# Optimization experiments

Measured on AMD Instinct MI355X. Metric: run time of the kernel, lower is better.

Reference implementation:

```python
import jax, jax.numpy as jnp
import numpy as np

B, T, D, H, HS = 256, 256, 384, 6, 64  # batch, seq (=block_size), n_embd, n_heads, head_size


def setup_inputs() -> dict:
    key = jax.random.key(0)
    k0, k1, k2 = jax.random.split(key, 3)
    x = jax.random.normal(k0, (B, T, D), dtype=jnp.float32)
    # per-head qkv weights, stacked: [H, n_embd, 3*head_size] (x @ W layout)
    W_qkv = jax.random.normal(k1, (H, D, 3 * HS), dtype=jnp.float32) * 0.02
    W_out = jax.random.normal(k2, (H * HS, D), dtype=jnp.float32) * 0.02
    b_out = jnp.zeros((D,), dtype=jnp.float32)
    return {"x": x, "W_qkv": W_qkv, "W_out": W_out, "b_out": b_out}


def reference(x, W_qkv, W_out, b_out):
    # Eval-mode (dropout disabled). Vectorized over heads instead of the
    # original Python loop; identical math per head.
    b, t, d = x.shape
    h, hs3 = W_qkv.shape[0], W_qkv.shape[2]
    hs = hs3 // 3
    qkv = jnp.einsum('btd,hde->bhte', x, W_qkv)  # [B,H,T,3*HS]
    q, k, v = jnp.split(qkv, 3, axis=-1)  # each [B,H,T,HS]
    scale = 1.0 / jnp.sqrt(jnp.asarray(hs, dtype=x.dtype))
    wei = jnp.einsum('bhte,bhse->bhts', q, k) * scale  # [B,H,T,T]
    causal = jnp.tril(jnp.ones((t, t), dtype=bool))
    wei = jnp.where(causal, wei, -jnp.inf)
    wei = jax.nn.softmax(wei, axis=-1)
    out = jnp.einsum('bhts,bhse->bhte', wei, v)  # [B,H,T,HS]
    out = out.transpose(0, 2, 1, 3).reshape(b, t, h * hs)  # concat heads
    return out @ W_out + b_out
```

## Files before the change

### kernel.cpp

```cpp
#include <hip/hip_runtime.h>


typedef __attribute__((ext_vector_type(8))) short short8;
typedef __attribute__((ext_vector_type(4))) float f32x4;

#define NBATCH 256
#define NT 256
#define ND 384
#define NH 6
#define NHS 64

__device__ __forceinline__ unsigned short f2bf(float f) {
  unsigned int u = __float_as_uint(f);
  u += 0x7fffu + ((u >> 16) & 1u);
  return (unsigned short)(u >> 16);
}

__device__ __forceinline__ unsigned int cvtpk(float lo, float hi) {
  unsigned int r;
  asm("v_cvt_pk_bf16_f32 %0, %1, %2" : "=v"(r) : "v"(lo), "v"(hi));
  return r;
}

__device__ __forceinline__ ushort4 pack4(f32x4 v) {
  union { uint2 u; ushort4 s; } r;
  r.u.x = cvtpk(v[0], v[1]);
  r.u.y = cvtpk(v[2], v[3]);
  return r.s;
}

__device__ __forceinline__ void gload16(const void* g, void* l) {
  __builtin_amdgcn_global_load_lds(
      (const __attribute__((address_space(1))) void*)g,
      (__attribute__((address_space(3))) void*)l, 16, 0, 0);
}

__global__ __launch_bounds__(256) void prep_all(const float* __restrict__ x,
                                                const float* __restrict__ Wqkv,
                                                const float* __restrict__ Wout,
                                                unsigned short* __restrict__ xb,
                                                unsigned short* __restrict__ Wqt,
                                                unsigned short* __restrict__ Wot) {
  const int bid = blockIdx.x;
  if (bid < 12288) {
    size_t i = ((size_t)bid * 256 + threadIdx.x) * 8;
    float4 a = *reinterpret_cast<const float4*>(&x[i]);
    float4 b = *reinterpret_cast<const float4*>(&x[i + 4]);
    ushort4 lo, hi;
    lo.x = f2bf(a.x); lo.y = f2bf(a.y); lo.z = f2bf(a.z); lo.w = f2bf(a.w);
    hi.x = f2bf(b.x); hi.y = f2bf(b.y); hi.z = f2bf(b.z); hi.w = f2bf(b.w);
    *reinterpret_cast<ushort4*>(&xb[i]) = lo;
    *reinterpret_cast<ushort4*>(&xb[i + 4]) = hi;
  } else if (bid < 14016) {
    int idx = (bid - 12288) * 256 + threadIdx.x;
    int h = idx / (192 * ND);
    int rem = idx % (192 * ND);
    int e = rem / ND;
    int d = rem % ND;
    float v = Wqkv[((size_t)h * ND + d) * 192 + e];
    if (e < 64) v *= 0.125f * 1.44269504088896340736f;
    Wqt[idx] = f2bf(v);
  } else {
    int idx = (bid - 14016) * 256 + threadIdx.x;
    int n = idx / ND;
    int k = idx % ND;
    Wot[idx] = f2bf(Wout[(size_t)k * ND + n]);
  }
}

__global__ __launch_bounds__(256, 2) void qkv_gemm(const unsigned short* __restrict__ xb,
                                                   const unsigned short* __restrict__ Wt,
                                                   unsigned short* __restrict__ Qb,
                                                   unsigned short* __restrict__ Kb,
                                                   unsigned short* __restrict__ Vtb) {
  __shared__ __align__(16) unsigned short As[2][128 * 64];
  __shared__ __align__(16) unsigned short Bs[2][192 * 64];
  const int tid = threadIdx.x;
  const int lane = tid & 63, w = tid >> 6;
  const int l15 = lane & 15, lg = lane >> 4;
  const int wm = w >> 1, wn = w & 1;

  const int bid = blockIdx.x;
  const int xcd = bid & 7, pos = bid >> 3;
  const int h = pos % 6;
  const int mt = xcd * 64 + pos / 6;
  const int m0 = mt * 128;
  const unsigned short* Wh = Wt + (size_t)h * 192 * ND;

  f32x4 acc[4][6];
#pragma unroll
  for (int i = 0; i < 4; i++)
#pragma unroll
    for (int j = 0; j < 6; j++) acc[i][j] = (f32x4){0.f, 0.f, 0.f, 0.f};

  int arow[4], acsw[4], brow[6], bcsw[6];
#pragma unroll
  for (int j = 0; j < 4; j++) {
    int chunk = j * 256 + tid;
    arow[j] = chunk >> 3;
    acsw[j] = (chunk & 7) ^ (arow[j] & 7);
  }
#pragma unroll
  for (int j = 0; j < 6; j++) {
    int chunk = j * 256 + tid;
    brow[j] = chunk >> 3;
    bcsw[j] = (chunk & 7) ^ (brow[j] & 7);
  }

#define STAGE(nb, k0)                                                              \
  do {                                                                             \
    _Pragma("unroll") for (int j = 0; j < 4; j++)                                  \
        gload16(&xb[(size_t)(m0 + arow[j]) * ND + (k0) + acsw[j] * 8],             \
                &As[nb][(j * 256 + w * 64) * 8]);                                  \
    _Pragma("unroll") for (int j = 0; j < 6; j++)                                  \
        gload16(&Wh[(size_t)brow[j] * ND + (k0) + bcsw[j] * 8],                    \
                &Bs[nb][(j * 256 + w * 64) * 8]);                                  \
  } while (0)

  STAGE(0, 0);
  __syncthreads();

  int cur = 0;
  for (int kt = 0; kt < 6; ++kt) {
    if (kt < 5) STAGE(cur ^ 1, (kt + 1) * 64);
    short8 af[4][2], bf[6][2];
#pragma unroll
    for (int mi = 0; mi < 4; mi++) {
      const int row = wm * 64 + mi * 16 + l15;
#pragma unroll
      for (int kk = 0; kk < 2; kk++)
        af[mi][kk] = *reinterpret_cast<const short8*>(
            &As[cur][row * 64 + (((kk * 4 + lg) ^ (row & 7)) * 8)]);
    }
#pragma unroll
    for (int ni = 0; ni < 6; ni++) {
      const int row = wn * 96 + ni * 16 + l15;
#pragma unroll
      for (int kk = 0; kk < 2; kk++)
        bf[ni][kk] = *reinterpret_cast<const short8*>(
            &Bs[cur][row * 64 + (((kk * 4 + lg) ^ (row & 7)) * 8)]);
    }
#pragma unroll
    for (int kk = 0; kk < 2; kk++)
#pragma unroll
      for (int mi = 0; mi < 4; mi++)
#pragma unroll
        for (int ni = 0; ni < 6; ni++)
          acc[mi][ni] = __builtin_amdgcn_mfma_f32_16x16x32_bf16(af[mi][kk], bf[ni][kk], acc[mi][ni], 0, 0, 0);
    __syncthreads();
    cur ^= 1;
  }

  const int b = m0 >> 8, t0 = m0 & 255;
  const size_t bh = (size_t)b * NH + h;
#pragma unroll
  for (int mi = 0; mi < 4; mi++)
#pragma unroll
    for (int ni = 0; ni < 6; ni++) {
      const int col = wn * 96 + ni * 16 + l15;
      const int p = col >> 6, e = col & 63;
      const int mr = wm * 64 + mi * 16 + lg * 4;
      if (p == 2) {
        *reinterpret_cast<ushort4*>(&Vtb[(bh * 64 + e) * NT + t0 + mr]) = pack4(acc[mi][ni]);
      } else {
        unsigned short* dst = (p == 0) ? Qb : Kb;
        size_t base = (bh * NT + t0 + mr) * 64 + e;
#pragma unroll
        for (int r = 0; r < 4; r++) dst[base + (size_t)r * 64] = f2bf(acc[mi][ni][r]);
      }
    }
#undef STAGE
}

__global__ __launch_bounds__(256, 2) void attn_fwd(const unsigned short* __restrict__ Qb,
                                                   const unsigned short* __restrict__ Kb,
                                                   const unsigned short* __restrict__ Vtb,
                                                   unsigned short* __restrict__ AO) {
  __shared__ __align__(16) unsigned short Ks[256 * 64];
  __shared__ __align__(16) unsigned short Plds[4][32 * 64];
  const int bh = blockIdx.x;
  const int tid = threadIdx.x;
  const int w = tid >> 6, lane = tid & 63;
  const int l15 = lane & 15, lg = lane >> 4;
  const unsigned short* Qh = Qb + (size_t)bh * NT * 64;
  const unsigned short* Kh = Kb + (size_t)bh * NT * 64;
  const unsigned short* Vh = Vtb + (size_t)bh * 64 * NT;
  unsigned short* P = Plds[w];
  const int swz = (l15 & 7) << 3;

  short8 qf[2][2];
  {
    const int q0 = w * 32;
#pragma unroll
    for (int mi = 0; mi < 2; mi++)
#pragma unroll
      for (int kb = 0; kb < 2; kb++)
        qf[mi][kb] = *reinterpret_cast<const short8*>(
            &Qh[(size_t)(q0 + mi * 16 + l15) * 64 + kb * 32 + lg * 8]);
  }

#pragma unroll
  for (int j = 0; j < 8; j++) {
    const int c = j * 256 + tid;
    const int row = c >> 3, cc = c & 7;
    gload16(&Kh[(size_t)row * 64 + ((cc ^ (row & 7)) * 8)], &Ks[c * 8]);
  }
  __syncthreads();

  const int b = bh / NH, h = bh % NH;

#pragma unroll
  for (int pass = 0; pass < 2; ++pass) {
    const int qt = pass ? (7 - w) : w;
    const int q0 = qt * 32;

    if (pass) {
#pragma unroll
      for (int mi = 0; mi < 2; mi++)
#pragma unroll
        for (int kb = 0; kb < 2; kb++)
          qf[mi][kb] = *reinterpret_cast<const short8*>(
              &Qh[(size_t)(q0 + mi * 16 + l15) * 64 + kb * 32 + lg * 8]);
    }

    f32x4 ot[4][2];
#pragma unroll
    for (int i = 0; i < 4; i++)
#pragma unroll
      for (int j = 0; j < 2; j++) ot[i][j] = (f32x4){0.f, 0.f, 0.f, 0.f};
    float mrun[2] = {-3e38f, -3e38f}, lsum[2] = {0.f, 0.f};

    const int nch = (qt >> 1) + 1;
    for (int ch = 0; ch < nch; ++ch) {
      const int kv0 = ch * 64;
      short8 va[4][2];
#pragma unroll
      for (int erb = 0; erb < 4; erb++) {
        const int row = erb * 16 + l15;
        va[erb][0] = *reinterpret_cast<const short8*>(&Vh[(size_t)row * NT + kv0 + lg * 8]);
        va[erb][1] = *reinterpret_cast<const short8*>(&Vh[(size_t)row * NT + kv0 + 32 + lg * 8]);
      }

      f32x4 st[4][2];
#pragma unroll
      for (int i = 0; i < 4; i++)
#pragma unroll
        for (int j = 0; j < 2; j++) st[i][j] = (f32x4){0.f, 0.f, 0.f, 0.f};
      __builtin_amdgcn_s_setprio(1);
#pragma unroll
      for (int ni = 0; ni < 4; ni++) {
        const int row = kv0 + ni * 16 + l15;
        const short8 kf0 = *reinterpret_cast<const short8*>(
            &Ks[row * 64 + ((lg ^ (row & 7)) * 8)]);
        const short8 kf1 = *reinterpret_cast<const short8*>(
            &Ks[row * 64 + (((4 + lg) ^ (row & 7)) * 8)]);
#pragma unroll
        for (int mi = 0; mi < 2; mi++) {
          st[ni][mi] = __builtin_amdgcn_mfma_f32_16x16x32_bf16(kf0, qf[mi][0], st[ni][mi], 0, 0, 0);
          st[ni][mi] = __builtin_amdgcn_mfma_f32_16x16x32_bf16(kf1, qf[mi][1], st[ni][mi], 0, 0, 0);
        }
      }
      __builtin_amdgcn_s_setprio(0);

      if (ch == nch - 1) {
#pragma unroll
        for (int ni = 0; ni < 4; ni++)
#pragma unroll
          for (int mi = 0; mi < 2; mi++)
#pragma unroll
            for (int r = 0; r < 4; r++)
              if (kv0 + ni * 16 + lg * 4 + r > q0 + mi * 16 + l15)
                st[ni][mi][r] = -1e30f;
      }

#pragma unroll
      for (int mi = 0; mi < 2; mi++) {
        float tmax = st[0][mi][0];
#pragma unroll
        for (int ni = 0; ni < 4; ni++)
#pragma unroll
          for (int r = 0; r < 4; r++) tmax = fmaxf(tmax, st[ni][mi][r]);
        tmax = fmaxf(tmax, __shfl_xor(tmax, 16));
        tmax = fmaxf(tmax, __shfl_xor(tmax, 32));
        if (__any(tmax > mrun[mi] + 8.0f)) {
          const float mnew = fmaxf(mrun[mi], tmax);
          const float corr = __builtin_amdgcn_exp2f(mrun[mi] - mnew);
          lsum[mi] *= corr;
#pragma unroll
          for (int erb = 0; erb < 4; erb++)
#pragma unroll
            for (int r = 0; r < 4; r++) ot[erb][mi][r] *= corr;
          mrun[mi] = mnew;
        }
        const float mref = mrun[mi];
        float ls = 0.f;
        const int prow = (mi * 16 + l15) * 64;
#pragma unroll
        for (int ni = 0; ni < 4; ni++) {
          const float p0 = __builtin_amdgcn_exp2f(st[ni][mi][0] - mref);
          const float p1 = __builtin_amdgcn_exp2f(st[ni][mi][1] - mref);
          const float p2 = __builtin_amdgcn_exp2f(st[ni][mi][2] - mref);
          const float p3 = __builtin_amdgcn_exp2f(st[ni][mi][3] - mref);
          ls += (p0 + p1) + (p2 + p3);
          uint2 wv;
          wv.x = cvtpk(p0, p1);
          wv.y = cvtpk(p2, p3);
          *reinterpret_cast<uint2*>(&P[prow + ((ni * 16 + lg * 4) ^ swz)]) = wv;
        }
        ls += __shfl_xor(ls, 16);
        ls += __shfl_xor(ls, 32);
        lsum[mi] += ls;
      }

      short8 pb[2][2];
#pragma unroll
      for (int kk = 0; kk < 2; kk++)
#pragma unroll
        for (int mi = 0; mi < 2; mi++)
          pb[kk][mi] = *reinterpret_cast<const short8*>(
              &P[(mi * 16 + l15) * 64 + ((kk * 32 + lg * 8) ^ swz)]);
      __builtin_amdgcn_s_setprio(1);
#pragma unroll
      for (int erb = 0; erb < 4; erb++)
#pragma unroll
        for (int mi = 0; mi < 2; mi++) {
          ot[erb][mi] = __builtin_amdgcn_mfma_f32_16x16x32_bf16(va[erb][0], pb[0][mi], ot[erb][mi], 0, 0, 0);
          ot[erb][mi] = __builtin_amdgcn_mfma_f32_16x16x32_bf16(va[erb][1], pb[1][mi], ot[erb][mi], 0, 0, 0);
        }
      __builtin_amdgcn_s_setprio(0);
    }

#pragma unroll
    for (int mi = 0; mi < 2; mi++) {
      const float rl = 1.0f / lsum[mi];
      const int q = q0 + mi * 16 + l15;
#pragma unroll
      for (int erb = 0; erb < 4; erb++) {
        f32x4 v;
#pragma unroll
        for (int r = 0; r < 4; r++) v[r] = ot[erb][mi][r] * rl;
        *reinterpret_cast<ushort4*>(&AO[((size_t)(b * NT + q)) * ND + h * 64 + erb * 16 + lg * 4]) =
            pack4(v);
      }
    }
  }
}

__global__ __launch_bounds__(256, 2) void out_gemm(const unsigned short* __restrict__ AO,
                                                   const unsigned short* __restrict__ Wot,
                                                   const float* __restrict__ bout,
                                                   float* __restrict__ out) {
  __shared__ __align__(16) unsigned short As[2][128 * 64];
  __shared__ __align__(16) unsigned short Bs[2][192 * 64];
  const int tid = threadIdx.x;
  const int lane = tid & 63, w = tid >> 6;
  const int l15 = lane & 15, lg = lane >> 4;
  const int wm = w >> 1, wn = w & 1;

  const int bid = blockIdx.x;
  const int xcd = bid & 7, pos = bid >> 3;
  const int n0 = (pos & 1) * 192;
  const int m0 = (xcd * 64 + (pos >> 1)) * 128;
  const unsigned short* Wh = Wot + (size_t)n0 * ND;

  f32x4 acc[4][6];
#pragma unroll
  for (int i = 0; i < 4; i++)
#pragma unroll
    for (int j = 0; j < 6; j++) acc[i][j] = (f32x4){0.f, 0.f, 0.f, 0.f};

  int arow[4], acsw[4], brow[6], bcsw[6];
#pragma unroll
  for (int j = 0; j < 4; j++) {
    int chunk = j * 256 + tid;
    arow[j] = chunk >> 3;
    acsw[j] = (chunk & 7) ^ (arow[j] & 7);
  }
#pragma unroll
  for (int j = 0; j < 6; j++) {
    int chunk = j * 256 + tid;
    brow[j] = chunk >> 3;
    bcsw[j] = (chunk & 7) ^ (brow[j] & 7);
  }

#define STAGE(nb, k0)                                                              \
  do {                                                                             \
    _Pragma("unroll") for (int j = 0; j < 4; j++)                                  \
        gload16(&AO[(size_t)(m0 + arow[j]) * ND + (k0) + acsw[j] * 8],             \
                &As[nb][(j * 256 + w * 64) * 8]);                                  \
    _Pragma("unroll") for (int j = 0; j < 6; j++)                                  \
        gload16(&Wh[(size_t)brow[j] * ND + (k0) + bcsw[j] * 8],                    \
                &Bs[nb][(j * 256 + w * 64) * 8]);                                  \
  } while (0)

  STAGE(0, 0);
  __syncthreads();

  int cur = 0;
  for (int kt = 0; kt < 6; ++kt) {
    if (kt < 5) STAGE(cur ^ 1, (kt + 1) * 64);
    short8 af[4][2], bf[6][2];
#pragma unroll
    for (int mi = 0; mi < 4; mi++) {
      const int row = wm * 64 + mi * 16 + l15;
#pragma unroll
      for (int kk = 0; kk < 2; kk++)
        af[mi][kk] = *reinterpret_cast<const short8*>(
            &As[cur][row * 64 + (((kk * 4 + lg) ^ (row & 7)) * 8)]);
    }
#pragma unroll
    for (int ni = 0; ni < 6; ni++) {
      const int row = wn * 96 + ni * 16 + l15;
#pragma unroll
      for (int kk = 0; kk < 2; kk++)
        bf[ni][kk] = *reinterpret_cast<const short8*>(
            &Bs[cur][row * 64 + (((kk * 4 + lg) ^ (row & 7)) * 8)]);
    }
#pragma unroll
    for (int kk = 0; kk < 2; kk++)
#pragma unroll
      for (int mi = 0; mi < 4; mi++)
#pragma unroll
        for (int ni = 0; ni < 6; ni++)
          acc[mi][ni] = __builtin_amdgcn_mfma_f32_16x16x32_bf16(af[mi][kk], bf[ni][kk], acc[mi][ni], 0, 0, 0);
    __syncthreads();
    cur ^= 1;
  }

#pragma unroll
  for (int mi = 0; mi < 4; mi++)
#pragma unroll
    for (int ni = 0; ni < 6; ni++) {
      const int c = n0 + wn * 96 + ni * 16 + l15;
      const int mr = m0 + wm * 64 + mi * 16 + lg * 4;
      const float bb = bout[c];
#pragma unroll
      for (int r = 0; r < 4; r++) out[(size_t)(mr + r) * ND + c] = acc[mi][ni][r] + bb;
    }
#undef STAGE
}

extern "C" void kernel_launch(void* const* d_in, const int* in_sizes, int n_in,
                              void* d_out, int out_size, void* d_ws, size_t ws_size,
                              hipStream_t stream) {
  const float* x = (const float*)d_in[0];
  const float* Wqkv = (const float*)d_in[1];
  const float* Wout = (const float*)d_in[2];
  const float* bout = (const float*)d_in[3];

  char* ws = (char*)d_ws;
  const size_t SZ = (size_t)NBATCH * NH * NT * NHS * 2;
  unsigned short* Qb  = (unsigned short*)(ws);
  unsigned short* Kb  = (unsigned short*)(ws + SZ);
  unsigned short* Vtb = (unsigned short*)(ws + 2 * SZ);
  unsigned short* AO  = (unsigned short*)(ws + 3 * SZ);
  unsigned short* xb  = AO;
  unsigned short* Wqt = (unsigned short*)(ws + 4 * SZ);
  unsigned short* Wot = (unsigned short*)(ws + 4 * SZ + 884736);

  prep_all<<<14592, 256, 0, stream>>>(x, Wqkv, Wout, xb, Wqt, Wot);
  qkv_gemm<<<3072, 256, 0, stream>>>(xb, Wqt, Qb, Kb, Vtb);
  attn_fwd<<<NBATCH * NH, 256, 0, stream>>>(Qb, Kb, Vtb, AO);
  out_gemm<<<1024, 256, 0, stream>>>(AO, Wot, bout, (float*)d_out);
}
```

Before: 191.6 us.

## Fuse fp32-to-bf16 conversion of x into the QKV GEMM A-tile loads

Removes the separate pass that converted x to bf16 in the workspace. The QKV GEMM now reads fp32 x directly into registers, converts with packed bf16 instructions, and writes the swizzled tile to LDS after the MFMAs, keeping the double-buffered prefetch. This avoids writing and re-reading a bf16 copy of x (about 50MB of fp32 read plus 25MB written and re-read). In exchange, the GEMM reads fp32 x once per head, six times in total with L2 reuse, and uses more registers plus VALU/LDS-store work per tile.

```diff
diff --git a/kernel.cpp b/kernel.cpp
--- a/kernel.cpp
+++ b/kernel.cpp
@@ -35,24 +35,13 @@
       (__attribute__((address_space(3))) void*)l, 16, 0, 0);
 }
 
-__global__ __launch_bounds__(256) void prep_all(const float* __restrict__ x,
-                                                const float* __restrict__ Wqkv,
-                                                const float* __restrict__ Wout,
-                                                unsigned short* __restrict__ xb,
-                                                unsigned short* __restrict__ Wqt,
-                                                unsigned short* __restrict__ Wot) {
+__global__ __launch_bounds__(256) void prep_w(const float* __restrict__ Wqkv,
+                                              const float* __restrict__ Wout,
+                                              unsigned short* __restrict__ Wqt,
+                                              unsigned short* __restrict__ Wot) {
   const int bid = blockIdx.x;
-  if (bid < 12288) {
-    size_t i = ((size_t)bid * 256 + threadIdx.x) * 8;
-    float4 a = *reinterpret_cast<const float4*>(&x[i]);
-    float4 b = *reinterpret_cast<const float4*>(&x[i + 4]);
-    ushort4 lo, hi;
-    lo.x = f2bf(a.x); lo.y = f2bf(a.y); lo.z = f2bf(a.z); lo.w = f2bf(a.w);
-    hi.x = f2bf(b.x); hi.y = f2bf(b.y); hi.z = f2bf(b.z); hi.w = f2bf(b.w);
-    *reinterpret_cast<ushort4*>(&xb[i]) = lo;
-    *reinterpret_cast<ushort4*>(&xb[i + 4]) = hi;
-  } else if (bid < 14016) {
-    int idx = (bid - 12288) * 256 + threadIdx.x;
+  if (bid < 1728) {
+    int idx = bid * 256 + threadIdx.x;
     int h = idx / (192 * ND);
     int rem = idx % (192 * ND);
     int e = rem / ND;
@@ -61,14 +50,14 @@
     if (e < 64) v *= 0.125f * 1.44269504088896340736f;
     Wqt[idx] = f2bf(v);
   } else {
-    int idx = (bid - 14016) * 256 + threadIdx.x;
+    int idx = (bid - 1728) * 256 + threadIdx.x;
     int n = idx / ND;
     int k = idx % ND;
     Wot[idx] = f2bf(Wout[(size_t)k * ND + n]);
   }
 }
 
-__global__ __launch_bounds__(256, 2) void qkv_gemm(const unsigned short* __restrict__ xb,
+__global__ __launch_bounds__(256, 2) void qkv_gemm(const float* __restrict__ x,
                                                    const unsigned short* __restrict__ Wt,
                                                    unsigned short* __restrict__ Qb,
                                                    unsigned short* __restrict__ Kb,
@@ -93,12 +82,12 @@
 #pragma unroll
     for (int j = 0; j < 6; j++) acc[i][j] = (f32x4){0.f, 0.f, 0.f, 0.f};
 
-  int arow[4], acsw[4], brow[6], bcsw[6];
+  int arow[4], acc8[4], brow[6], bcsw[6];
 #pragma unroll
   for (int j = 0; j < 4; j++) {
     int chunk = j * 256 + tid;
     arow[j] = chunk >> 3;
-    acsw[j] = (chunk & 7) ^ (arow[j] & 7);
+    acc8[j] = (chunk & 7) ^ (arow[j] & 7);
   }
 #pragma unroll
   for (int j = 0; j < 6; j++) {
@@ -107,22 +96,47 @@
     bcsw[j] = (chunk & 7) ^ (brow[j] & 7);
   }
 
-#define STAGE(nb, k0)                                                              \
+  float4 areg[4][2];
+
+#define A_LOAD(k0)                                                                 \
   do {                                                                             \
-    _Pragma("unroll") for (int j = 0; j < 4; j++)                                  \
-        gload16(&xb[(size_t)(m0 + arow[j]) * ND + (k0) + acsw[j] * 8],             \
-                &As[nb][(j * 256 + w * 64) * 8]);                                  \
+    _Pragma("unroll") for (int j = 0; j < 4; j++) {                                \
+      const float* ap = &x[(size_t)(m0 + arow[j]) * ND + (k0) + acc8[j] * 8];      \
+      areg[j][0] = *reinterpret_cast<const float4*>(ap);                           \
+      areg[j][1] = *reinterpret_cast<const float4*>(ap + 4);                       \
+    }                                                                              \
+  } while (0)
+
+#define A_WRITE(nb)                                                                \
+  do {                                                                             \
+    _Pragma("unroll") for (int j = 0; j < 4; j++) {                                \
+      uint4 v;                                                                     \
+      v.x = cvtpk(areg[j][0].x, areg[j][0].y);                                     \
+      v.y = cvtpk(areg[j][0].z, areg[j][0].w);                                     \
+      v.z = cvtpk(areg[j][1].x, areg[j][1].y);                                     \
+      v.w = cvtpk(areg[j][1].z, areg[j][1].w);                                     \
+      *reinterpret_cast<uint4*>(&As[nb][(j * 256 + tid) * 8]) = v;                 \
+    }                                                                              \
+  } while (0)
+
+#define B_STAGE(nb, k0)                                                            \
+  do {                                                                             \
     _Pragma("unroll") for (int j = 0; j < 6; j++)                                  \
         gload16(&Wh[(size_t)brow[j] * ND + (k0) + bcsw[j] * 8],                    \
                 &Bs[nb][(j * 256 + w * 64) * 8]);                                  \
   } while (0)
 
-  STAGE(0, 0);
+  A_LOAD(0);
+  B_STAGE(0, 0);
+  A_WRITE(0);
   __syncthreads();
 
   int cur = 0;
   for (int kt = 0; kt < 6; ++kt) {
-    if (kt < 5) STAGE(cur ^ 1, (kt + 1) * 64);
+    if (kt < 5) {
+      A_LOAD((kt + 1) * 64);
+      B_STAGE(cur ^ 1, (kt + 1) * 64);
+    }
     short8 af[4][2], bf[6][2];
 #pragma unroll
     for (int mi = 0; mi < 4; mi++) {
@@ -147,6 +161,7 @@
 #pragma unroll
         for (int ni = 0; ni < 6; ni++)
           acc[mi][ni] = __builtin_amdgcn_mfma_f32_16x16x32_bf16(af[mi][kk], bf[ni][kk], acc[mi][ni], 0, 0, 0);
+    if (kt < 5) A_WRITE(cur ^ 1);
     __syncthreads();
     cur ^= 1;
   }
@@ -169,7 +184,9 @@
         for (int r = 0; r < 4; r++) dst[base + (size_t)r * 64] = f2bf(acc[mi][ni][r]);
       }
     }
-#undef STAGE
+#undef A_LOAD
+#undef A_WRITE
+#undef B_STAGE
 }
 
 __global__ __launch_bounds__(256, 2) void attn_fwd(const unsigned short* __restrict__ Qb,
@@ -454,12 +471,11 @@
   unsigned short* Kb  = (unsigned short*)(ws + SZ);
   unsigned short* Vtb = (unsigned short*)(ws + 2 * SZ);
   unsigned short* AO  = (unsigned short*)(ws + 3 * SZ);
-  unsigned short* xb  = AO;
   unsigned short* Wqt = (unsigned short*)(ws + 4 * SZ);
   unsigned short* Wot = (unsigned short*)(ws + 4 * SZ + 884736);
 
-  prep_all<<<14592, 256, 0, stream>>>(x, Wqkv, Wout, xb, Wqt, Wot);
-  qkv_gemm<<<3072, 256, 0, stream>>>(xb, Wqt, Qb, Kb, Vtb);
+  prep_w<<<2304, 256, 0, stream>>>(Wqkv, Wout, Wqt, Wot);
+  qkv_gemm<<<3072, 256, 0, stream>>>(x, Wqt, Qb, Kb, Vtb);
   attn_fwd<<<NBATCH * NH, 256, 0, stream>>>(Qb, Kb, Vtb, AO);
   out_gemm<<<1024, 256, 0, stream>>>(AO, Wot, bout, (float*)d_out);
 }
```

After: 224.5 us. 17.2% more time.
